# Performance work log

Hardware: AMD Instinct MI355X
Metric: run time of the kernel (lower is better)

Reference implementation:

```python
import jax, jax.numpy as jnp
import numpy as np

EPSILON = 0.01        # temperature
DIST_THRESH = 0.2
NUM_ITERS = 8         # sparse_rebalance_iters (== num_iters here)
TOPK = 64             # topk_support
NEG_INF = -1e9


def setup_inputs() -> dict:
    key = jax.random.key(0)
    k1, k2, k3 = jax.random.split(key, 3)
    B, N, M, D = 4, 4096, 4096, 128
    return {
        "source_feats": jax.random.normal(k1, (B, N, D), dtype=jnp.float32),
        "source_locs": jax.random.uniform(k2, (B, N, 2), dtype=jnp.float32),
        "target_locs": jax.random.uniform(k3, (B, M, 2), dtype=jnp.float32),
        "source_valid_mask": jnp.ones((B, N), dtype=bool),
        "target_valid_mask": jnp.ones((B, M), dtype=bool),
    }


def _sinkhorn_attn(source_locs, target_locs, source_valid_mask, target_valid_mask):
    # pairwise squared distances: [B, M, N]
    diff = target_locs[:, :, None, :] - source_locs[:, None, :, :]
    dist_sq = jnp.sum(diff * diff, axis=-1)
    log_k = -dist_sq / (EPSILON + 1e-8)
    valid = (dist_sq < DIST_THRESH ** 2)
    valid = valid & source_valid_mask[:, None, :] & target_valid_mask[:, :, None]

    B, M, N = valid.shape
    topk = min(TOPK, N)
    if topk < N:
        masked_log_k = jnp.where(valid, log_k, NEG_INF)
        _, topk_idx = jax.lax.top_k(masked_log_k, topk)  # [B, M, topk]
        support = jnp.zeros_like(valid).at[
            jnp.arange(B)[:, None, None], jnp.arange(M)[None, :, None], topk_idx
        ].set(True)
        valid = valid & support

    log_k = jnp.where(valid, log_k, NEG_INF)

    v = jnp.zeros((B, 1, N), dtype=log_k.dtype)
    u = jnp.zeros((B, M, 1), dtype=log_k.dtype)
    for _ in range(NUM_ITERS):
        u = -jax.nn.logsumexp(log_k + v, axis=2, keepdims=True)
        v = -jax.nn.logsumexp(log_k + u, axis=1, keepdims=True)
        v = jnp.where(source_valid_mask[:, None, :], v, 0.0)

    attn = jnp.exp(log_k + u + v)              # [B, M, N]
    has_source = valid.any(axis=-1, keepdims=True)  # [B, M, 1]
    return attn, has_source


def reference(source_feats, source_locs, target_locs, source_valid_mask, target_valid_mask):
    attn, has_source = _sinkhorn_attn(source_locs, target_locs,
                                      source_valid_mask, target_valid_mask)
    target_feats = jnp.einsum('bmn,bnd->bmd', attn, source_feats)
    target_feats = target_feats * target_valid_mask[:, :, None].astype(target_feats.dtype)
    target_feats = target_feats * has_source.astype(target_feats.dtype)
    return target_feats
```

## Files before the change

kernel.cpp:

```cpp
#include <hip/hip_runtime.h>
#include <math.h>

#define B 4
#define N 4096
#define M 4096
#define D 128
#define K 64
#define BT 256
#define WPB 4
#define RPW 4
#define CAP 768
#define CUTCAP 128
#define PC 128
#define SCAP 2048
#define EPS_DENOM 0.01000001f
#define THRESH2 0.04f
#define GC 16

__global__ __launch_bounds__(1024) void k_sort(const float* __restrict__ slocs,
        const float* __restrict__ tlocs,
        float4* __restrict__ sPack, float4* __restrict__ tPack,
        int* __restrict__ cellStart,
        int* __restrict__ colcnt, int* __restrict__ E, int* __restrict__ R,
        float* __restrict__ extraF, float* __restrict__ cs){
    __shared__ int hist[256], startS[256], fill[256], wtot[4];
    __shared__ float2 loc[N];
    __shared__ unsigned short scell[N];
    const int blk = blockIdx.x, tid = threadIdx.x;
    const bool tgt = blk >= B;
    const int b = tgt ? (blk - B) : blk;
    const int lane = tid & 63, w = tid >> 6;
    const float2* slp = (const float2*)((tgt ? tlocs : slocs) + (size_t)b * N * 2);
    float4* outPack = (tgt ? tPack : sPack) + (size_t)b * N;

    if (!tgt){
        for (int i = tid; i < N; i += 1024){
            colcnt[b * N + i] = 0;
            cs[b * N + i] = 1.0f;
        }
        if (b == 0){
            if (tid < B){ E[tid] = 0; R[tid] = 0; }
            if (tid < B * D) extraF[tid] = 0.f;
        }
    }

    if (tid < 256){ hist[tid] = 0; fill[tid] = 0; }
    __syncthreads();
    for (int i = tid; i < N; i += 1024){
        float2 p = slp[i];
        int cx = min(GC - 1, max(0, (int)(p.x * (float)GC)));
        int cy = min(GC - 1, max(0, (int)(p.y * (float)GC)));
        int cell = cy * GC + cx;
        loc[i] = p; scell[i] = (unsigned short)cell;
        atomicAdd(&hist[cell], 1);
    }
    __syncthreads();
    int hv = (tid < 256) ? hist[tid] : 0;
    int pre = hv;
    #pragma unroll
    for (int o = 1; o < 64; o <<= 1){ int t2 = __shfl_up(pre, o, 64); if (lane >= o) pre += t2; }
    if (tid < 256 && lane == 63) wtot[w] = pre;
    __syncthreads();
    if (tid < 256){
        int off = 0;
        for (int i = 0; i < w; ++i) off += wtot[i];
        int st = off + pre - hv;
        startS[tid] = st;
        if (!tgt) cellStart[b * 257 + tid] = st;
    }
    if (!tgt && tid == 0) cellStart[b * 257 + 256] = N;
    __syncthreads();
    for (int i = tid; i < N; i += 1024){
        int cell = scell[i];
        int pos = startS[cell] + atomicAdd(&fill[cell], 1);
        float2 p = loc[i];
        outPack[pos] = make_float4(p.x, p.y, __int_as_float(i), 0.f);
    }
}

__global__ __launch_bounds__(BT, 4) void k_build(const float4* __restrict__ sPack,
        const int* __restrict__ cellStart, const float4* __restrict__ tPack,
        float* __restrict__ elkA, int* __restrict__ idxA, int* __restrict__ cnt,
        int* __restrict__ colcnt, float* __restrict__ cscElk, int* __restrict__ cscRow,
        int* __restrict__ R){
    __shared__ int cs[257];
    __shared__ float2 sxy[SCAP];
    __shared__ int    sid[SCAP];
    __shared__ unsigned short cj[WPB][CAP];
    __shared__ int   hist[WPB][64];
    __shared__ float cutd[WPB][CUTCAP];
    __shared__ int   cutn[WPB][CUTCAP];
    __shared__ float4 rowT[16];
    __shared__ int gB[16], gL[16], lB[16];
    __shared__ int stot;

    const int bid  = blockIdx.x;
    const int sb   = (bid & 7) * 128 + (bid >> 3);
    const int b    = sb >> 8;
    const int s00  = (sb & 255) * (WPB * RPW);
    const int tid  = threadIdx.x;
    const int w    = tid >> 6;
    const int lane = tid & 63;
    const unsigned long long pmask = (lane == 0) ? 0ull : ((1ull << lane) - 1);
    const float4* sp = sPack + (size_t)b * N;
    const float4* tp = tPack + (size_t)b * M;

    for (int i = tid; i < 257; i += BT) cs[i] = cellStart[b * 257 + i];
    if (tid < 16) rowT[tid] = tp[s00 + tid];
    __syncthreads();

    float txmin = 1e9f, txmax = -1e9f, tymin = 1e9f, tymax = -1e9f;
    #pragma unroll
    for (int i = 0; i < 16; ++i){
        float4 t = rowT[i];
        txmin = fminf(txmin, t.x); txmax = fmaxf(txmax, t.x);
        tymin = fminf(tymin, t.y); tymax = fmaxf(tymax, t.y);
    }
    const int bcy0 = max(0, (int)floorf((tymin - 0.2f) * (float)GC - 0.001f));
    const int bcy1 = min(GC - 1, (int)floorf((tymax + 0.2f) * (float)GC + 0.001f));
    const int ncy  = bcy1 - bcy0 + 1;
    if (tid < ncy && tid < 16){
        int cy = bcy0 + tid;
        float rowLo = cy * 0.0625f, rowHi = rowLo + 0.0625f;
        float dymin = fmaxf(0.f, fmaxf(rowLo - tymax, tymin - rowHi));
        float dxm = sqrtf(fmaxf(THRESH2 - dymin * dymin + 1e-5f, 0.f));
        int cx0 = max(0, (int)floorf((txmin - dxm) * (float)GC - 0.001f));
        int cx1 = min(GC - 1, (int)floorf((txmax + dxm) * (float)GC + 0.001f));
        int s = cs[cy * GC + cx0], e = cs[cy * GC + cx1 + 1];
        gB[tid] = s; gL[tid] = e - s;
    }
    __syncthreads();
    if (tid == 0){
        if (ncy > 16) stot = SCAP + 1;
        else {
            int acc = 0;
            for (int i = 0; i < ncy; ++i){ lB[i] = acc; acc += gL[i]; }
            stot = acc;
        }
    }
    __syncthreads();
    const bool staged = (stot <= SCAP);
    if (staged){
        for (int i = 0; i < ncy; ++i){
            int s = gB[i], len = gL[i], l0 = lB[i];
            for (int j = tid; j < len; j += BT){
                float4 q = sp[s + j];
                sxy[l0 + j] = make_float2(q.x, q.y);
                sid[l0 + j] = __float_as_int(q.z);
            }
        }
    }
    __syncthreads();

    for (int r = 0; r < RPW; ++r){
        const float4 t  = rowT[w * RPW + r];
        const float tx  = t.x;
        const float ty  = t.y;
        const int m     = __float_as_int(t.z);
        const int rowid = b * M + m;

        hist[w][lane] = 0;

        const int cy0 = max(0, (int)floorf((ty - 0.2f) * (float)GC - 0.001f));
        const int cy1 = min(GC - 1, (int)floorf((ty + 0.2f) * (float)GC + 0.001f));

        int c = 0;
        for (int cy = cy0; cy <= cy1; ++cy){
            float rowLo = cy * 0.0625f, rowHi = rowLo + 0.0625f;
            float dymin = fmaxf(0.f, fmaxf(rowLo - ty, ty - rowHi));
            float dxm = sqrtf(fmaxf(THRESH2 - dymin * dymin + 1e-5f, 0.f));
            int cx0 = max(0, (int)floorf((tx - dxm) * (float)GC - 0.001f));
            int cx1 = min(GC - 1, (int)floorf((tx + dxm) * (float)GC + 0.001f));
            int s = cs[cy * GC + cx0], e = cs[cy * GC + cx1 + 1];
            int len = e - s;
            int base_l = staged ? (lB[cy - bcy0] + (s - gB[cy - bcy0])) : s;
            for (int j0 = 0; j0 < len; j0 += 64){
                int i = j0 + lane;
                bool valid = i < len;
                int lp = base_l + i;
                float d2 = 1e9f;
                if (valid){
                    float qx, qy;
                    if (staged){ float2 q = sxy[lp]; qx = q.x; qy = q.y; }
                    else       { float4 q = sp[lp];  qx = q.x; qy = q.y; }
                    float dx = __fsub_rn(tx, qx);
                    float dy = __fsub_rn(ty, qy);
                    d2 = __fadd_rn(__fmul_rn(dx, dx), __fmul_rn(dy, dy));
                }
                bool in = valid && (d2 < THRESH2);
                unsigned long long ml = __ballot(in);
                if (in){
                    int p = c + __popcll(ml & pmask);
                    if (p < CAP) cj[w][p] = (unsigned short)lp;
                    atomicAdd(&hist[w][min((int)(d2 * 1600.0f), 63)], 1);
                }
                c += __popcll(ml);
            }
        }
        const int ctot = min(c, CAP);

        int h = hist[w][lane];
        int pre = h;
        #pragma unroll
        for (int o = 1; o < 64; o <<= 1){
            int t2 = __shfl_up(pre, o, 64);
            if (lane >= o) pre += t2;
        }
        int cutB = 64, q = 0;
        if (c > K){
            unsigned long long ge = __ballot(pre >= K);
            int fb = __ffsll((long long)ge) - 1;
            cutB = fb;
            q = K - __shfl(pre - h, fb, 64);
        }

        int base = 0, cutc = 0;
        for (int i0 = 0; i0 < ctot; i0 += 64){
            int i = i0 + lane;
            bool valid = i < ctot;
            float d2 = 1e9f; int n = 0;
            if (valid){
                int lp = cj[w][i];
                float qx, qy;
                if (staged){ float2 q = sxy[lp]; qx = q.x; qy = q.y; n = sid[lp]; }
                else       { float4 q = sp[lp];  qx = q.x; qy = q.y; n = __float_as_int(q.z); }
                float dx = __fsub_rn(tx, qx);
                float dy = __fsub_rn(ty, qy);
                d2 = __fadd_rn(__fmul_rn(dx, dx), __fmul_rn(dy, dy));
            }
            int bk = valid ? min((int)(d2 * 1600.0f), 63) : 64;
            bool low = valid && (bk < cutB);
            unsigned long long ml = __ballot(low);
            if (low){
                int p = base + __popcll(ml & pmask);
                float e = expf(-(d2 / EPS_DENOM));
                elkA[(size_t)rowid * K + p] = e;
                idxA[(size_t)rowid * K + p] = n;
                int bn = b * N + n;
                int slot = atomicAdd(&colcnt[bn], 1);
                if (slot < PC){
                    cscElk[(size_t)bn * PC + slot] = e;
                    cscRow[(size_t)bn * PC + slot] = rowid;
                }
            }
            base += __popcll(ml);
            if (cutB < 64){
                bool eq = valid && (bk == cutB);
                unsigned long long me = __ballot(eq);
                if (eq){
                    int p = cutc + __popcll(me & pmask);
                    if (p < CUTCAP){ cutd[w][p] = d2; cutn[w][p] = n; }
                }
                cutc += __popcll(me);
            }
        }

        if (c > K){
            int cc = min(cutc, CUTCAP);
            for (int i0 = 0; i0 < CUTCAP; i0 += 64){
                int i = i0 + lane;
                bool sel = false; float d2i = 0.f; int ni = 0;
                if (i < cc){
                    d2i = cutd[w][i]; ni = cutn[w][i];
                    int rank = 0;
                    for (int j = 0; j < cc; ++j){
                        float dj = cutd[w][j]; int nj = cutn[w][j];
                        rank += (dj < d2i) || (dj == d2i && nj < ni);
                    }
                    sel = rank < q;
                }
                unsigned long long ms = __ballot(sel);
                if (sel){
                    int p = base + __popcll(ms & pmask);
                    float e = expf(-(d2i / EPS_DENOM));
                    elkA[(size_t)rowid * K + p] = e;
                    idxA[(size_t)rowid * K + p] = ni;
                    int bn = b * N + ni;
                    int slot = atomicAdd(&colcnt[bn], 1);
                    if (slot < PC){
                        cscElk[(size_t)bn * PC + slot] = e;
                        cscRow[(size_t)bn * PC + slot] = rowid;
                    }
                }
                base += __popcll(ms);
                if (i0 + 64 >= cc) break;
            }
            if (lane == 0) cnt[rowid] = K;
        } else {
            if (lane == 0){
                cnt[rowid] = c;
                if (c == 0) atomicAdd(&R[b], 1);
            }
        }
    }
}

__global__ __launch_bounds__(256) void k_prep(const int* __restrict__ colcnt,
        int* __restrict__ E, const float* __restrict__ feats, float* __restrict__ extraF){
    int t = blockIdx.x * blockDim.x + threadIdx.x;
    int lane = t & 63, b = t >> 12;
    int cc = colcnt[t];
    unsigned long long em = __ballot(cc == 0);
    if (lane == 0 && em) atomicAdd(&E[b], __popcll(em));
    if (cc == 0){
        for (int d = 0; d < D; ++d)
            atomicAdd(&extraF[b * D + d], feats[(size_t)t * D + d]);
    }
}

__global__ __launch_bounds__(256) void kA(const float* __restrict__ elkA,
        const int* __restrict__ idxA, const int* __restrict__ cnt,
        const float* __restrict__ cs, const int* __restrict__ E, float* __restrict__ eu){
    int t = blockIdx.x * blockDim.x + threadIdx.x;
    int W = t >> 6, lane = t & 63;
    for (int rr = 0; rr < 4; ++rr){
        int rid = W * 4 + rr;
        int b = rid >> 12;
        int c = cnt[rid];
        float s = 0.f;
        if (lane < c){
            int ix = (b << 12) + idxA[(size_t)rid * K + lane];
            s = elkA[(size_t)rid * K + lane] / cs[ix];
        }
        #pragma unroll
        for (int o = 32; o; o >>= 1) s += __shfl_xor(s, o, 64);
        int Eb = E[b];
        if (c == 0 && Eb == 0){
            if (lane == 0) eu[rid] = 0.f;
        } else {
            if (Eb > 0) s += (float)Eb;
            if (lane == 0) eu[rid] = 1.0f / s;
        }
    }
}

__global__ __launch_bounds__(256) void kB(const float* __restrict__ cscElk,
        const int* __restrict__ cscRow, const int* __restrict__ colcnt,
        const float* __restrict__ eu, const int* __restrict__ R, float* __restrict__ cs){
    int t = blockIdx.x * blockDim.x + threadIdx.x;
    int W = t >> 6, lane = t & 63;
    for (int rr = 0; rr < 4; ++rr){
        int cid = W * 4 + rr;
        int b = cid >> 12;
        int cc = min(colcnt[cid], PC);
        float s = 0.f;
        for (int p = lane; p < cc; p += 64)
            s += cscElk[(size_t)cid * PC + p] * eu[cscRow[(size_t)cid * PC + p]];
        #pragma unroll
        for (int o = 32; o; o >>= 1) s += __shfl_xor(s, o, 64);
        if (lane == 0)
            cs[cid] = s + (float)R[b];
    }
}

__global__ __launch_bounds__(128) void k_out(const float* __restrict__ feats,
        const float* __restrict__ elkA, const int* __restrict__ idxA,
        const int* __restrict__ cnt, const float* __restrict__ eu,
        const float* __restrict__ cs, const float* __restrict__ extraF,
        const float4* __restrict__ tPack, float* __restrict__ out){
    __shared__ float att[K];
    __shared__ int   sidx[K];
    int bid = blockIdx.x;
    int sg  = (bid & 7) * 2048 + (bid >> 3);
    int b   = sg >> 12;
    int srt = sg & 4095;
    int m   = __float_as_int(tPack[(size_t)b * M + srt].z);
    int rid = (b << 12) + m;
    int tid = threadIdx.x;
    int c = cnt[rid];
    if (tid < K){
        float a = 0.f; int ix = 0;
        if (tid < c){
            ix = idxA[(size_t)rid * K + tid];
            a = elkA[(size_t)rid * K + tid] * eu[rid] / cs[(b << 12) + ix];
        }
        att[tid] = a; sidx[tid] = ix;
    }
    __syncthreads();
    float acc = 0.f;
    if (c > 0){
        acc = extraF[b * D + tid];
        for (int k = 0; k < c; ++k)
            acc += att[k] * feats[((size_t)((b << 12) + sidx[k])) * D + tid];
    }
    out[(size_t)rid * D + tid] = acc;
}

extern "C" void kernel_launch(void* const* d_in, const int* in_sizes, int n_in,
                              void* d_out, int out_size, void* d_ws, size_t ws_size,
                              hipStream_t stream){
    const float* feats = (const float*)d_in[0];
    const float* slocs = (const float*)d_in[1];
    const float* tlocs = (const float*)d_in[2];
    float* out = (float*)d_out;

    char* w = (char*)d_ws;
    size_t off = 0;
    auto carve = [&](size_t bytes) -> void* {
        void* p = w + off;
        off += (bytes + 255) & ~(size_t)255;
        return p;
    };
    float* elkA    = (float*)carve((size_t)B * M * K * 4);
    int*   idxA    = (int*)  carve((size_t)B * M * K * 4);
    float* cscElk  = (float*)carve((size_t)B * N * PC * 4);
    int*   cscRow  = (int*)  carve((size_t)B * N * PC * 4);
    int*   cnt     = (int*)  carve((size_t)B * M * 4);
    int*   colcnt  = (int*)  carve((size_t)B * N * 4);
    float* eu      = (float*)carve((size_t)B * M * 4);
    float* cs      = (float*)carve((size_t)B * N * 4);
    int*   E       = (int*)  carve(B * 4);
    int*   R       = (int*)  carve(B * 4);
    float* extraF  = (float*)carve((size_t)B * D * 4);
    float4* sPack  = (float4*)carve((size_t)B * N * 16);
    float4* tPack  = (float4*)carve((size_t)B * M * 16);
    int*   cellStart = (int*)carve((size_t)B * 257 * 4);

    k_sort<<<2 * B, 1024, 0, stream>>>(slocs, tlocs, sPack, tPack, cellStart,
                                       colcnt, E, R, extraF, cs);
    k_build<<<B * M / (WPB * RPW), BT, 0, stream>>>(sPack, cellStart, tPack,
            elkA, idxA, cnt, colcnt, cscElk, cscRow, R);
    k_prep<<<(B * N) / 256, 256, 0, stream>>>(colcnt, E, feats, extraF);
    for (int it = 0; it < 8; ++it){
        kA<<<B * M / 16, 256, 0, stream>>>(elkA, idxA, cnt, cs, E, eu);
        kB<<<B * N / 16, 256, 0, stream>>>(cscElk, cscRow, colcnt, eu, R, cs);
    }
    k_out<<<B * M, D, 0, stream>>>(feats, elkA, idxA, cnt, eu, cs, extraF, tPack, out);
}
```

Measured before the change: 259.0 us.

## Index rows and columns in spatially sorted order, pack original ids

Result: faster. 248.3 us (-4.1%).

```diff
diff --git a/kernel.cpp b/kernel.cpp
--- a/kernel.cpp
+++ b/kernel.cpp
@@ -12,7 +12,7 @@
 #define CAP 768
 #define CUTCAP 128
 #define PC 128
-#define SCAP 2048
+#define SCAP 1536
 #define EPS_DENOM 0.01000001f
 #define THRESH2 0.04f
 #define GC 16
@@ -78,7 +78,7 @@
     }
 }
 
-__global__ __launch_bounds__(BT, 4) void k_build(const float4* __restrict__ sPack,
+__global__ __launch_bounds__(BT, 5) void k_build(const float4* __restrict__ sPack,
         const int* __restrict__ cellStart, const float4* __restrict__ tPack,
         float* __restrict__ elkA, int* __restrict__ idxA, int* __restrict__ cnt,
         int* __restrict__ colcnt, float* __restrict__ cscElk, int* __restrict__ cscRow,
@@ -146,18 +146,18 @@
             for (int j = tid; j < len; j += BT){
                 float4 q = sp[s + j];
                 sxy[l0 + j] = make_float2(q.x, q.y);
-                sid[l0 + j] = __float_as_int(q.z);
+                sid[l0 + j] = ((s + j) << 16) | __float_as_int(q.z);
             }
         }
     }
     __syncthreads();
 
     for (int r = 0; r < RPW; ++r){
+        const int srt   = s00 + w * RPW + r;
+        const int srid  = b * M + srt;
         const float4 t  = rowT[w * RPW + r];
         const float tx  = t.x;
         const float ty  = t.y;
-        const int m     = __float_as_int(t.z);
-        const int rowid = b * M + m;
 
         hist[w][lane] = 0;
 
@@ -218,12 +218,13 @@
         for (int i0 = 0; i0 < ctot; i0 += 64){
             int i = i0 + lane;
             bool valid = i < ctot;
-            float d2 = 1e9f; int n = 0;
+            float d2 = 1e9f; int pk = 0;
             if (valid){
                 int lp = cj[w][i];
                 float qx, qy;
-                if (staged){ float2 q = sxy[lp]; qx = q.x; qy = q.y; n = sid[lp]; }
-                else       { float4 q = sp[lp];  qx = q.x; qy = q.y; n = __float_as_int(q.z); }
+                if (staged){ float2 q = sxy[lp]; qx = q.x; qy = q.y; pk = sid[lp]; }
+                else       { float4 q = sp[lp];  qx = q.x; qy = q.y;
+                             pk = (lp << 16) | __float_as_int(q.z); }
                 float dx = __fsub_rn(tx, qx);
                 float dy = __fsub_rn(ty, qy);
                 d2 = __fadd_rn(__fmul_rn(dx, dx), __fmul_rn(dy, dy));
@@ -234,13 +235,13 @@
             if (low){
                 int p = base + __popcll(ml & pmask);
                 float e = expf(-(d2 / EPS_DENOM));
-                elkA[(size_t)rowid * K + p] = e;
-                idxA[(size_t)rowid * K + p] = n;
-                int bn = b * N + n;
+                elkA[(size_t)srid * K + p] = e;
+                idxA[(size_t)srid * K + p] = pk;
+                int bn = (b << 12) + (pk >> 16);
                 int slot = atomicAdd(&colcnt[bn], 1);
                 if (slot < PC){
                     cscElk[(size_t)bn * PC + slot] = e;
-                    cscRow[(size_t)bn * PC + slot] = rowid;
+                    cscRow[(size_t)bn * PC + slot] = srid;
                 }
             }
             base += __popcll(ml);
@@ -249,7 +250,7 @@
                 unsigned long long me = __ballot(eq);
                 if (eq){
                     int p = cutc + __popcll(me & pmask);
-                    if (p < CUTCAP){ cutd[w][p] = d2; cutn[w][p] = n; }
+                    if (p < CUTCAP){ cutd[w][p] = d2; cutn[w][p] = pk; }
                 }
                 cutc += __popcll(me);
             }
@@ -265,7 +266,7 @@
                     int rank = 0;
                     for (int j = 0; j < cc; ++j){
                         float dj = cutd[w][j]; int nj = cutn[w][j];
-                        rank += (dj < d2i) || (dj == d2i && nj < ni);
+                        rank += (dj < d2i) || (dj == d2i && (nj & 0xFFFF) < (ni & 0xFFFF));
                     }
                     sel = rank < q;
                 }
@@ -273,22 +274,22 @@
                 if (sel){
                     int p = base + __popcll(ms & pmask);
                     float e = expf(-(d2i / EPS_DENOM));
-                    elkA[(size_t)rowid * K + p] = e;
-                    idxA[(size_t)rowid * K + p] = ni;
-                    int bn = b * N + ni;
+                    elkA[(size_t)srid * K + p] = e;
+                    idxA[(size_t)srid * K + p] = ni;
+                    int bn = (b << 12) + (ni >> 16);
                     int slot = atomicAdd(&colcnt[bn], 1);
                     if (slot < PC){
                         cscElk[(size_t)bn * PC + slot] = e;
-                        cscRow[(size_t)bn * PC + slot] = rowid;
+                        cscRow[(size_t)bn * PC + slot] = srid;
                     }
                 }
                 base += __popcll(ms);
                 if (i0 + 64 >= cc) break;
             }
-            if (lane == 0) cnt[rowid] = K;
+            if (lane == 0) cnt[srid] = K;
         } else {
             if (lane == 0){
-                cnt[rowid] = c;
+                cnt[srid] = c;
                 if (c == 0) atomicAdd(&R[b], 1);
             }
         }
@@ -296,15 +297,17 @@
 }
 
 __global__ __launch_bounds__(256) void k_prep(const int* __restrict__ colcnt,
-        int* __restrict__ E, const float* __restrict__ feats, float* __restrict__ extraF){
+        int* __restrict__ E, const float* __restrict__ feats,
+        const float4* __restrict__ sPack, float* __restrict__ extraF){
     int t = blockIdx.x * blockDim.x + threadIdx.x;
     int lane = t & 63, b = t >> 12;
     int cc = colcnt[t];
     unsigned long long em = __ballot(cc == 0);
     if (lane == 0 && em) atomicAdd(&E[b], __popcll(em));
     if (cc == 0){
+        int orig = __float_as_int(sPack[t].z);
         for (int d = 0; d < D; ++d)
-            atomicAdd(&extraF[b * D + d], feats[(size_t)t * D + d]);
+            atomicAdd(&extraF[b * D + d], feats[((size_t)((b << 12) + orig)) * D + d]);
     }
 }
 
@@ -319,8 +322,8 @@
         int c = cnt[rid];
         float s = 0.f;
         if (lane < c){
-            int ix = (b << 12) + idxA[(size_t)rid * K + lane];
-            s = elkA[(size_t)rid * K + lane] / cs[ix];
+            int pk = idxA[(size_t)rid * K + lane];
+            s = elkA[(size_t)rid * K + lane] / cs[(b << 12) + (pk >> 16)];
         }
         #pragma unroll
         for (int o = 32; o; o >>= 1) s += __shfl_xor(s, o, 64);
@@ -365,25 +368,26 @@
     int b   = sg >> 12;
     int srt = sg & 4095;
     int m   = __float_as_int(tPack[(size_t)b * M + srt].z);
-    int rid = (b << 12) + m;
     int tid = threadIdx.x;
-    int c = cnt[rid];
+    int c = cnt[sg];
     if (tid < K){
-        float a = 0.f; int ix = 0;
+        float a = 0.f; int pk = 0;
         if (tid < c){
-            ix = idxA[(size_t)rid * K + tid];
-            a = elkA[(size_t)rid * K + tid] * eu[rid] / cs[(b << 12) + ix];
-        }
-        att[tid] = a; sidx[tid] = ix;
+            pk = idxA[(size_t)sg * K + tid];
+            a = elkA[(size_t)sg * K + tid] * eu[sg] / cs[(b << 12) + (pk >> 16)];
+        }
+        att[tid] = a; sidx[tid] = pk;
     }
     __syncthreads();
     float acc = 0.f;
     if (c > 0){
         acc = extraF[b * D + tid];
-        for (int k = 0; k < c; ++k)
-            acc += att[k] * feats[((size_t)((b << 12) + sidx[k])) * D + tid];
-    }
-    out[(size_t)rid * D + tid] = acc;
+        for (int k = 0; k < c; ++k){
+            int orig = sidx[k] & 0xFFFF;
+            acc += att[k] * feats[((size_t)((b << 12) + orig)) * D + tid];
+        }
+    }
+    out[((size_t)((b << 12) + m)) * D + tid] = acc;
 }
 
 extern "C" void kernel_launch(void* const* d_in, const int* in_sizes, int n_in,
@@ -420,7 +424,7 @@
                                        colcnt, E, R, extraF, cs);
     k_build<<<B * M / (WPB * RPW), BT, 0, stream>>>(sPack, cellStart, tPack,
             elkA, idxA, cnt, colcnt, cscElk, cscRow, R);
-    k_prep<<<(B * N) / 256, 256, 0, stream>>>(colcnt, E, feats, extraF);
+    k_prep<<<(B * N) / 256, 256, 0, stream>>>(colcnt, E, feats, sPack, extraF);
     for (int it = 0; it < 8; ++it){
         kA<<<B * M / 16, 256, 0, stream>>>(elkA, idxA, cnt, cs, E, eu);
         kB<<<B * N / 16, 256, 0, stream>>>(cscElk, cscRow, colcnt, eu, R, cs);
```
